# Performance work log

Measured on AMD Instinct MI355X. Metric: run time of the kernel, lower is better.

The kernel has to match this reference:

```python
import jax, jax.numpy as jnp
import numpy as np


def _gcn_conv(x, W, b, src, dst, dinv, n_nodes):
    # x: [N, Cin], W: [Cin, Cout]. PyG GCNConv: transform then normalized aggregate.
    h = x @ W  # [N, Cout]
    norm = dinv[src] * dinv[dst]  # [E']
    msgs = h[src] * norm[:, None]  # gather + scale, [E', Cout]
    out = jax.ops.segment_sum(msgs, dst, num_segments=n_nodes)
    return out + b


def setup_inputs() -> dict:
    key = jax.random.key(0)
    k1, k2, k3, k4 = jax.random.split(key, 4)
    N, E, C = 100000, 1600000, 128
    x = jax.random.normal(k1, (N, C), dtype=jnp.float32)
    edge_index = jax.random.randint(k2, (2, E), 0, N, dtype=jnp.int32)
    # Glorot-ish scale for square layers
    s = 1.0 / np.sqrt(C)
    W1 = jax.random.normal(k3, (C, C), dtype=jnp.float32) * s
    W2 = jax.random.normal(k4, (C, C), dtype=jnp.float32) * s
    b1 = jnp.zeros((C,), dtype=jnp.float32)
    b2 = jnp.zeros((C,), dtype=jnp.float32)
    return {"x": x, "edge_index": edge_index, "W1": W1, "b1": b1, "W2": W2, "b2": b2}


def reference(x, edge_index, W1, b1, W2, b2):
    n_nodes = x.shape[0]
    # Add self-loops (PyG GCNConv default add_self_loops=True)
    loops = jnp.arange(n_nodes, dtype=edge_index.dtype)
    src = jnp.concatenate([edge_index[0], loops])
    dst = jnp.concatenate([edge_index[1], loops])
    # Symmetric normalization: deg^-1/2 with degree counted at destination
    deg = jax.ops.segment_sum(jnp.ones_like(dst, dtype=x.dtype), dst, num_segments=n_nodes)
    dinv = jnp.where(deg > 0, jax.lax.rsqrt(jnp.maximum(deg, 1e-12)), 0.0)

    h = _gcn_conv(x, W1, b1, src, dst, dinv, n_nodes)
    h = jax.nn.relu(h)
    out = _gcn_conv(h, W2, b2, src, dst, dinv, n_nodes)
    return out
```

## Files before the change

kernel.cpp:

```cpp
#include <hip/hip_runtime.h>

#define CDIM 128
#define BCAP 12288
#define LCAP 10240

typedef __bf16 v8bf __attribute__((ext_vector_type(8)));
typedef float  v4f  __attribute__((ext_vector_type(4)));

__device__ __forceinline__ unsigned short f2bf(float f) {
    unsigned int u = __float_as_uint(f);
    u += 0x7fffu + ((u >> 16) & 1u);
    return (unsigned short)(u >> 16);
}

__global__ __launch_bounds__(256) void k_init_bcur(int* __restrict__ bcur) {
    bcur[threadIdx.x] = threadIdx.x * BCAP;
}

__global__ __launch_bounds__(256) void k_bucket_scatter(const int* __restrict__ src,
                                                        const int* __restrict__ dst,
                                                        int* __restrict__ bcur,
                                                        unsigned int* __restrict__ pairs,
                                                        int E) {
    __shared__ int cnt[256];
    __shared__ int cur[256];
    int t = threadIdx.x;
    cnt[t] = 0;
    __syncthreads();
    int e0 = blockIdx.x * 4096;
    int ds[16];
#pragma unroll
    for (int j = 0; j < 16; j++) {
        int e = e0 + j * 256 + t;
        ds[j] = (e < E) ? dst[e] : -1;
        if (ds[j] >= 0) atomicAdd(&cnt[ds[j] >> 9], 1);
    }
    __syncthreads();
    int c = cnt[t];
    cur[t] = c ? atomicAdd(&bcur[t], c) : 0;
    __syncthreads();
#pragma unroll
    for (int j = 0; j < 16; j++) {
        if (ds[j] >= 0) {
            int e = e0 + j * 256 + t;
            int p = atomicAdd(&cur[ds[j] >> 9], 1);
            pairs[p] = ((unsigned)src[e] << 9) | ((unsigned)ds[j] & 511u);
        }
    }
}

__global__ __launch_bounds__(256) void k_bucket_csr(const unsigned int* __restrict__ pairs,
                                                    const int* __restrict__ bcur,
                                                    int* __restrict__ csr,
                                                    int* __restrict__ rowptr,
                                                    float* __restrict__ dinv,
                                                    int N, int E, int NB) {
    __shared__ int sscan[256];
    __shared__ int deg[512];
    __shared__ int pre[512];
    __shared__ int sums[256];
    __shared__ int csrbuf[LCAP];
    int b = blockIdx.x, t = threadIdx.x;

    int c = (t < NB) ? (bcur[t] - t * BCAP) : 0;
    sscan[t] = c;
    __syncthreads();
    for (int off = 1; off < 256; off <<= 1) {
        int v = (t >= off) ? sscan[t - off] : 0;
        __syncthreads();
        sscan[t] += v;
        __syncthreads();
    }
    int cnt   = bcur[b] - b * BCAP;
    if (cnt > LCAP) cnt = LCAP;
    int gbase = sscan[b] - cnt;
    int nb0   = b << 9;

    deg[t] = 0; deg[t + 256] = 0;
    __syncthreads();
    for (int i = t; i < cnt; i += 256)
        atomicAdd(&deg[pairs[b * BCAP + i] & 511u], 1);
    __syncthreads();

    int d0 = deg[2 * t], d1 = deg[2 * t + 1];
    sums[t] = d0 + d1;
    __syncthreads();
    for (int off = 1; off < 256; off <<= 1) {
        int v = (t >= off) ? sums[t - off] : 0;
        __syncthreads();
        sums[t] += v;
        __syncthreads();
    }
    int eb = sums[t] - (d0 + d1);
    pre[2 * t]     = eb;
    pre[2 * t + 1] = eb + d0;
    __syncthreads();

    for (int l = t; l < 512; l += 256) {
        int g = nb0 + l;
        if (g < N) {
            rowptr[g] = gbase + pre[l];
            dinv[g]   = rsqrtf((float)(deg[l] + 1));
        }
    }
    if (b == 0 && t == 0) rowptr[N] = E;
    __syncthreads();

    for (int i = t; i < cnt; i += 256) {
        unsigned int p = pairs[b * BCAP + i];
        int l = (int)(p & 511u);
        int pos = atomicAdd(&pre[l], 1);
        csrbuf[pos] = (int)(p >> 9);
    }
    __syncthreads();

    for (int i = t; i < cnt; i += 256)
        csr[gbase + i] = csrbuf[i];
}

template<int INBF16>
__global__ __launch_bounds__(256) void k_gemm(const void* __restrict__ Xv,
                                              const float* __restrict__ W,
                                              const float* __restrict__ dinv,
                                              unsigned short* __restrict__ Hb,
                                              int N) {
    __shared__ char sX[64 * 256];
    __shared__ char sW[128 * 256];
    const int tid  = threadIdx.x;
    const int row0 = blockIdx.x * 64;

    if (INBF16) {
        const uint4* Xb = (const uint4*)Xv + (size_t)row0 * 16;
#pragma unroll
        for (int i = 0; i < 4; i++) {
            int q   = i * 256 + tid;
            int row = q >> 4;
            int c   = q & 15;
            uint4 v = make_uint4(0u, 0u, 0u, 0u);
            if (row0 + row < N) v = Xb[q];
            int addr = row * 256 + (((c ^ (row & 7)) << 4));
            *(uint4*)(sX + addr) = v;
        }
    } else {
        const float4* Xb = (const float4*)Xv + (size_t)row0 * 32;
#pragma unroll
        for (int i = 0; i < 8; i++) {
            int q   = i * 256 + tid;
            int row = q >> 5;
            int k4  = q & 31;
            float4 v = make_float4(0.f, 0.f, 0.f, 0.f);
            if (row0 + row < N) v = Xb[q];
            unsigned int lo = (unsigned int)f2bf(v.x) | ((unsigned int)f2bf(v.y) << 16);
            unsigned int hi = (unsigned int)f2bf(v.z) | ((unsigned int)f2bf(v.w) << 16);
            int chunk = k4 >> 1, half = k4 & 1;
            int addr = row * 256 + (((chunk ^ (row & 7)) << 4) | (half << 3));
            *(uint2*)(sX + addr) = make_uint2(lo, hi);
        }
    }
    {
        int kg = tid >> 5;
        int c0 = (tid & 31) * 4;
        unsigned int wp[4][8];
#pragma unroll
        for (int i = 0; i < 16; i++) {
            float4 v = *(const float4*)(W + (size_t)(kg * 16 + i) * CDIM + c0);
            unsigned short b0 = f2bf(v.x), b1 = f2bf(v.y), b2 = f2bf(v.z), b3 = f2bf(v.w);
            int ui = i >> 1;
            if ((i & 1) == 0) {
                wp[0][ui] = b0; wp[1][ui] = b1; wp[2][ui] = b2; wp[3][ui] = b3;
            } else {
                wp[0][ui] |= (unsigned int)b0 << 16;
                wp[1][ui] |= (unsigned int)b1 << 16;
                wp[2][ui] |= (unsigned int)b2 << 16;
                wp[3][ui] |= (unsigned int)b3 << 16;
            }
        }
#pragma unroll
        for (int j = 0; j < 4; j++) {
            int c = c0 + j;
            int base = c * 256;
            int a0 = base + ((((kg * 2) ^ (c & 7)) << 4));
            int a1 = base + ((((kg * 2 + 1) ^ (c & 7)) << 4));
            *(uint4*)(sW + a0) = make_uint4(wp[j][0], wp[j][1], wp[j][2], wp[j][3]);
            *(uint4*)(sW + a1) = make_uint4(wp[j][4], wp[j][5], wp[j][6], wp[j][7]);
        }
    }
    __syncthreads();

    const int l   = tid & 63;
    const int wv  = tid >> 6;
    const int ar  = l & 15;
    const int kg2 = l >> 4;

    v4f acc[8];
#pragma unroll
    for (int ct = 0; ct < 8; ct++) acc[ct] = (v4f){0.f, 0.f, 0.f, 0.f};

#pragma unroll
    for (int ks = 0; ks < 4; ks++) {
        int r = wv * 16 + ar;
        v8bf a = *(const v8bf*)(sX + r * 256 + (((ks * 4 + kg2) ^ (r & 7)) << 4));
#pragma unroll
        for (int ct = 0; ct < 8; ct++) {
            int c = ct * 16 + ar;
            v8bf b = *(const v8bf*)(sW + c * 256 + (((ks * 4 + kg2) ^ (c & 7)) << 4));
            acc[ct] = __builtin_amdgcn_mfma_f32_16x16x32_bf16(a, b, acc[ct], 0, 0, 0);
        }
    }

    int rbase = row0 + wv * 16 + kg2 * 4;
#pragma unroll
    for (int reg = 0; reg < 4; reg++) {
        int g = rbase + reg;
        if (g < N) {
            float di = dinv[g];
            unsigned short* orow = Hb + (size_t)g * CDIM;
#pragma unroll
            for (int ct = 0; ct < 8; ct++)
                orow[ct * 16 + ar] = f2bf(acc[ct][reg] * di);
        }
    }
}

template<int OUTBF16>
__global__ __launch_bounds__(256) void k_gather(const unsigned short* __restrict__ Hb,
                                                const int* __restrict__ csr,
                                                const int* __restrict__ rowptr,
                                                const float* __restrict__ dinv,
                                                const float* __restrict__ bias,
                                                void* __restrict__ outv,
                                                int N, int do_relu) {
    int t    = blockIdx.x * 256 + threadIdx.x;
    int n    = t >> 4;
    int lane = t & 15;
    if (n >= N) return;

    const uint4* base = (const uint4*)Hb;
    float acc[8] = {0.f, 0.f, 0.f, 0.f, 0.f, 0.f, 0.f, 0.f};

    auto accum = [&](uint4 u) {
        acc[0] += __uint_as_float(u.x << 16);
        acc[1] += __uint_as_float(u.x & 0xffff0000u);
        acc[2] += __uint_as_float(u.y << 16);
        acc[3] += __uint_as_float(u.y & 0xffff0000u);
        acc[4] += __uint_as_float(u.z << 16);
        acc[5] += __uint_as_float(u.z & 0xffff0000u);
        acc[6] += __uint_as_float(u.w << 16);
        acc[7] += __uint_as_float(u.w & 0xffff0000u);
    };

    int e  = rowptr[n];
    int e1 = rowptr[n + 1];

    accum(base[(size_t)n * 16 + lane]);

    for (; e + 8 <= e1; e += 8) {
        int s0 = csr[e],     s1 = csr[e + 1], s2 = csr[e + 2], s3 = csr[e + 3];
        int s4 = csr[e + 4], s5 = csr[e + 5], s6 = csr[e + 6], s7 = csr[e + 7];
        uint4 u0 = base[(size_t)s0 * 16 + lane];
        uint4 u1 = base[(size_t)s1 * 16 + lane];
        uint4 u2 = base[(size_t)s2 * 16 + lane];
        uint4 u3 = base[(size_t)s3 * 16 + lane];
        uint4 u4 = base[(size_t)s4 * 16 + lane];
        uint4 u5 = base[(size_t)s5 * 16 + lane];
        uint4 u6 = base[(size_t)s6 * 16 + lane];
        uint4 u7 = base[(size_t)s7 * 16 + lane];
        accum(u0); accum(u1); accum(u2); accum(u3);
        accum(u4); accum(u5); accum(u6); accum(u7);
    }
    for (; e + 2 <= e1; e += 2) {
        int s0 = csr[e], s1 = csr[e + 1];
        uint4 u0 = base[(size_t)s0 * 16 + lane];
        uint4 u1 = base[(size_t)s1 * 16 + lane];
        accum(u0); accum(u1);
    }
    if (e < e1) accum(base[(size_t)csr[e] * 16 + lane]);

    float di = dinv[n];
    const float* bp = bias + lane * 8;
    float o[8];
#pragma unroll
    for (int j = 0; j < 8; j++) o[j] = fmaf(acc[j], di, bp[j]);
    if (do_relu) {
#pragma unroll
        for (int j = 0; j < 8; j++) o[j] = fmaxf(o[j], 0.f);
    }

    if (OUTBF16) {
        uint4 u;
        u.x = (unsigned int)f2bf(o[0]) | ((unsigned int)f2bf(o[1]) << 16);
        u.y = (unsigned int)f2bf(o[2]) | ((unsigned int)f2bf(o[3]) << 16);
        u.z = (unsigned int)f2bf(o[4]) | ((unsigned int)f2bf(o[5]) << 16);
        u.w = (unsigned int)f2bf(o[6]) | ((unsigned int)f2bf(o[7]) << 16);
        ((uint4*)outv)[(size_t)n * 16 + lane] = u;
    } else {
        float* op = (float*)outv + (size_t)n * CDIM + lane * 8;
        *(float4*)(op)     = make_float4(o[0], o[1], o[2], o[3]);
        *(float4*)(op + 4) = make_float4(o[4], o[5], o[6], o[7]);
    }
}

extern "C" void kernel_launch(void* const* d_in, const int* in_sizes, int n_in,
                              void* d_out, int out_size, void* d_ws, size_t ws_size,
                              hipStream_t stream) {
    const float* x  = (const float*)d_in[0];
    const int*   ei = (const int*)d_in[1];
    const float* W1 = (const float*)d_in[2];
    const float* b1 = (const float*)d_in[3];
    const float* W2 = (const float*)d_in[4];
    const float* b2 = (const float*)d_in[5];
    float* out = (float*)d_out;

    const int N = in_sizes[0] / CDIM;
    const int E = in_sizes[1] / 2;
    const int* src = ei;
    const int* dst = ei + E;

    char* w = (char*)d_ws;
    unsigned short* Hb = (unsigned short*)w;  w += ((size_t)N * CDIM * 2 + 255) & ~255ull;
    float* dinv   = (float*)w;                w += ((size_t)N * 4 + 255) & ~255ull;
    int*   rowptr = (int*)w;                  w += ((size_t)(N + 1) * 4 + 255) & ~255ull;
    int*   bcur   = (int*)w;                  w += 1024;
    int*   csr    = (int*)w;                  w += ((size_t)E * 4 + 255) & ~255ull;
    unsigned int* pairs = (unsigned int*)w;
    unsigned short* Act = (unsigned short*)w;

    int NB = (N + 511) >> 9;
    int nA = (E + 4095) >> 12;
    int gb = (N + 63) / 64;
    int ga = (int)(((size_t)N * 16 + 255) / 256);

    k_init_bcur<<<1, 256, 0, stream>>>(bcur);
    k_bucket_scatter<<<nA, 256, 0, stream>>>(src, dst, bcur, pairs, E);
    k_bucket_csr<<<NB, 256, 0, stream>>>(pairs, bcur, csr, rowptr, dinv, N, E, NB);

    k_gemm<0><<<gb, 256, 0, stream>>>(x, W1, dinv, Hb, N);
    k_gather<1><<<ga, 256, 0, stream>>>(Hb, csr, rowptr, dinv, b1, Act, N, 1);

    k_gemm<1><<<gb, 256, 0, stream>>>(Act, W2, dinv, Hb, N);
    k_gather<0><<<ga, 256, 0, stream>>>(Hb, csr, rowptr, dinv, b2, out, N, 0);
}
```

Before: 217.1 us.

## Fuse layer-1 aggregation with layer-2 GEMM and pre-convert W2 to bf16

The first aggregation kernel now also performs the second layer's dense transform. Each 16-node block aggregates neighbours, applies bias and ReLU, stages the bf16 row in shared memory, and multiplies by a pre-swizzled bf16 copy of W2 with MFMA. The init kernel builds the W2 bf16 copy. This removes the intermediate activation write/read and one kernel launch. In exchange, every small block reloads the full 32KB W2 tile into shared memory, which raises L2 traffic and reduces occupancy for the latency-bound gather.

```diff
diff --git a/kernel.cpp b/kernel.cpp
--- a/kernel.cpp
+++ b/kernel.cpp
@@ -13,8 +13,25 @@
     return (unsigned short)(u >> 16);
 }
 
-__global__ __launch_bounds__(256) void k_init_bcur(int* __restrict__ bcur) {
-    bcur[threadIdx.x] = threadIdx.x * BCAP;
+__global__ __launch_bounds__(256) void k_init(int* __restrict__ bcur,
+                                              const float* __restrict__ W2,
+                                              uint4* __restrict__ W2bf) {
+    int t = threadIdx.x;
+    if (blockIdx.x == 0) {
+        bcur[t] = t * BCAP;
+        return;
+    }
+    int i  = (blockIdx.x - 1) * 256 + t;
+    int c  = i >> 4;
+    int ch = i & 15;
+    unsigned int p[4];
+#pragma unroll
+    for (int u = 0; u < 4; u++) {
+        float f0 = W2[(size_t)(ch * 8 + 2 * u) * CDIM + c];
+        float f1 = W2[(size_t)(ch * 8 + 2 * u + 1) * CDIM + c];
+        p[u] = (unsigned int)f2bf(f0) | ((unsigned int)f2bf(f1) << 16);
+    }
+    W2bf[(c * 256 + ((ch ^ (c & 7)) << 4)) >> 4] = make_uint4(p[0], p[1], p[2], p[3]);
 }
 
 __global__ __launch_bounds__(256) void k_bucket_scatter(const int* __restrict__ src,
@@ -118,8 +135,7 @@
         csr[gbase + i] = csrbuf[i];
 }
 
-template<int INBF16>
-__global__ __launch_bounds__(256) void k_gemm(const void* __restrict__ Xv,
+__global__ __launch_bounds__(256) void k_gemm(const float* __restrict__ X,
                                               const float* __restrict__ W,
                                               const float* __restrict__ dinv,
                                               unsigned short* __restrict__ Hb,
@@ -129,20 +145,8 @@
     const int tid  = threadIdx.x;
     const int row0 = blockIdx.x * 64;
 
-    if (INBF16) {
-        const uint4* Xb = (const uint4*)Xv + (size_t)row0 * 16;
-#pragma unroll
-        for (int i = 0; i < 4; i++) {
-            int q   = i * 256 + tid;
-            int row = q >> 4;
-            int c   = q & 15;
-            uint4 v = make_uint4(0u, 0u, 0u, 0u);
-            if (row0 + row < N) v = Xb[q];
-            int addr = row * 256 + (((c ^ (row & 7)) << 4));
-            *(uint4*)(sX + addr) = v;
-        }
-    } else {
-        const float4* Xb = (const float4*)Xv + (size_t)row0 * 32;
+    {
+        const float4* Xb = (const float4*)X + (size_t)row0 * 32;
 #pragma unroll
         for (int i = 0; i < 8; i++) {
             int q   = i * 256 + tid;
@@ -222,22 +226,29 @@
     }
 }
 
-template<int OUTBF16>
-__global__ __launch_bounds__(256) void k_gather(const unsigned short* __restrict__ Hb,
-                                                const int* __restrict__ csr,
-                                                const int* __restrict__ rowptr,
-                                                const float* __restrict__ dinv,
-                                                const float* __restrict__ bias,
-                                                void* __restrict__ outv,
-                                                int N, int do_relu) {
-    int t    = blockIdx.x * 256 + threadIdx.x;
-    int n    = t >> 4;
-    int lane = t & 15;
-    if (n >= N) return;
+__global__ __launch_bounds__(256) void k_gather_gemm(const unsigned short* __restrict__ Hb,
+                                                     const int* __restrict__ csr,
+                                                     const int* __restrict__ rowptr,
+                                                     const float* __restrict__ dinv,
+                                                     const float* __restrict__ bias,
+                                                     const uint4* __restrict__ W2bf,
+                                                     unsigned short* __restrict__ Hb2,
+                                                     int N) {
+    __shared__ char sA[16 * 256];
+    __shared__ char sW[128 * 256];
+    const int tid = threadIdx.x;
+    const int n0  = blockIdx.x * 16;
+
+#pragma unroll
+    for (int i = 0; i < 8; i++)
+        *(uint4*)(sW + ((i * 256 + tid) << 4)) = W2bf[i * 256 + tid];
+
+    int n    = n0 + (tid >> 4);
+    int lane = tid & 15;
+    int g    = tid >> 4;
 
     const uint4* base = (const uint4*)Hb;
     float acc[8] = {0.f, 0.f, 0.f, 0.f, 0.f, 0.f, 0.f, 0.f};
-
     auto accum = [&](uint4 u) {
         acc[0] += __uint_as_float(u.x << 16);
         acc[1] += __uint_as_float(u.x & 0xffff0000u);
@@ -249,11 +260,106 @@
         acc[7] += __uint_as_float(u.w & 0xffff0000u);
     };
 
+    uint4 row;
+    if (n < N) {
+        int e  = rowptr[n];
+        int e1 = rowptr[n + 1];
+        accum(base[(size_t)n * 16 + lane]);
+        for (; e + 8 <= e1; e += 8) {
+            int s0 = csr[e],     s1 = csr[e + 1], s2 = csr[e + 2], s3 = csr[e + 3];
+            int s4 = csr[e + 4], s5 = csr[e + 5], s6 = csr[e + 6], s7 = csr[e + 7];
+            uint4 u0 = base[(size_t)s0 * 16 + lane];
+            uint4 u1 = base[(size_t)s1 * 16 + lane];
+            uint4 u2 = base[(size_t)s2 * 16 + lane];
+            uint4 u3 = base[(size_t)s3 * 16 + lane];
+            uint4 u4 = base[(size_t)s4 * 16 + lane];
+            uint4 u5 = base[(size_t)s5 * 16 + lane];
+            uint4 u6 = base[(size_t)s6 * 16 + lane];
+            uint4 u7 = base[(size_t)s7 * 16 + lane];
+            accum(u0); accum(u1); accum(u2); accum(u3);
+            accum(u4); accum(u5); accum(u6); accum(u7);
+        }
+        for (; e + 2 <= e1; e += 2) {
+            int s0 = csr[e], s1 = csr[e + 1];
+            uint4 u0 = base[(size_t)s0 * 16 + lane];
+            uint4 u1 = base[(size_t)s1 * 16 + lane];
+            accum(u0); accum(u1);
+        }
+        if (e < e1) accum(base[(size_t)csr[e] * 16 + lane]);
+
+        float di = dinv[n];
+        const float* bp = bias + lane * 8;
+        float o[8];
+#pragma unroll
+        for (int j = 0; j < 8; j++) o[j] = fmaxf(fmaf(acc[j], di, bp[j]), 0.f);
+        row.x = (unsigned int)f2bf(o[0]) | ((unsigned int)f2bf(o[1]) << 16);
+        row.y = (unsigned int)f2bf(o[2]) | ((unsigned int)f2bf(o[3]) << 16);
+        row.z = (unsigned int)f2bf(o[4]) | ((unsigned int)f2bf(o[5]) << 16);
+        row.w = (unsigned int)f2bf(o[6]) | ((unsigned int)f2bf(o[7]) << 16);
+    } else {
+        row = make_uint4(0u, 0u, 0u, 0u);
+    }
+    *(uint4*)(sA + g * 256 + ((lane ^ (g & 7)) << 4)) = row;
+    __syncthreads();
+
+    const int l   = tid & 63;
+    const int wv  = tid >> 6;
+    const int ar  = l & 15;
+    const int kg2 = l >> 4;
+
+    v4f d0 = (v4f){0.f, 0.f, 0.f, 0.f};
+    v4f d1 = (v4f){0.f, 0.f, 0.f, 0.f};
+    const int c0 = (wv * 2) * 16 + ar;
+    const int c1 = (wv * 2 + 1) * 16 + ar;
+#pragma unroll
+    for (int ks = 0; ks < 4; ks++) {
+        int kc = ks * 4 + kg2;
+        v8bf a  = *(const v8bf*)(sA + ar * 256 + ((kc ^ (ar & 7)) << 4));
+        v8bf b0 = *(const v8bf*)(sW + c0 * 256 + ((kc ^ (c0 & 7)) << 4));
+        v8bf b1 = *(const v8bf*)(sW + c1 * 256 + ((kc ^ (c1 & 7)) << 4));
+        d0 = __builtin_amdgcn_mfma_f32_16x16x32_bf16(a, b0, d0, 0, 0, 0);
+        d1 = __builtin_amdgcn_mfma_f32_16x16x32_bf16(a, b1, d1, 0, 0, 0);
+    }
+#pragma unroll
+    for (int reg = 0; reg < 4; reg++) {
+        int gn = n0 + kg2 * 4 + reg;
+        if (gn < N) {
+            float di = dinv[gn];
+            unsigned short* orow = Hb2 + (size_t)gn * CDIM;
+            orow[c0] = f2bf(d0[reg] * di);
+            orow[c1] = f2bf(d1[reg] * di);
+        }
+    }
+}
+
+__global__ __launch_bounds__(256) void k_gather(const unsigned short* __restrict__ Hb,
+                                                const int* __restrict__ csr,
+                                                const int* __restrict__ rowptr,
+                                                const float* __restrict__ dinv,
+                                                const float* __restrict__ bias,
+                                                float* __restrict__ out,
+                                                int N) {
+    int t    = blockIdx.x * 256 + threadIdx.x;
+    int n    = t >> 4;
+    int lane = t & 15;
+    if (n >= N) return;
+
+    const uint4* base = (const uint4*)Hb;
+    float acc[8] = {0.f, 0.f, 0.f, 0.f, 0.f, 0.f, 0.f, 0.f};
+    auto accum = [&](uint4 u) {
+        acc[0] += __uint_as_float(u.x << 16);
+        acc[1] += __uint_as_float(u.x & 0xffff0000u);
+        acc[2] += __uint_as_float(u.y << 16);
+        acc[3] += __uint_as_float(u.y & 0xffff0000u);
+        acc[4] += __uint_as_float(u.z << 16);
+        acc[5] += __uint_as_float(u.z & 0xffff0000u);
+        acc[6] += __uint_as_float(u.w << 16);
+        acc[7] += __uint_as_float(u.w & 0xffff0000u);
+    };
+
     int e  = rowptr[n];
     int e1 = rowptr[n + 1];
-
     accum(base[(size_t)n * 16 + lane]);
-
     for (; e + 8 <= e1; e += 8) {
         int s0 = csr[e],     s1 = csr[e + 1], s2 = csr[e + 2], s3 = csr[e + 3];
         int s4 = csr[e + 4], s5 = csr[e + 5], s6 = csr[e + 6], s7 = csr[e + 7];
@@ -278,26 +384,14 @@
 
     float di = dinv[n];
     const float* bp = bias + lane * 8;
-    float o[8];
-#pragma unroll
-    for (int j = 0; j < 8; j++) o[j] = fmaf(acc[j], di, bp[j]);
-    if (do_relu) {
-#pragma unroll
-        for (int j = 0; j < 8; j++) o[j] = fmaxf(o[j], 0.f);
-    }
-
-    if (OUTBF16) {
-        uint4 u;
-        u.x = (unsigned int)f2bf(o[0]) | ((unsigned int)f2bf(o[1]) << 16);
-        u.y = (unsigned int)f2bf(o[2]) | ((unsigned int)f2bf(o[3]) << 16);
-        u.z = (unsigned int)f2bf(o[4]) | ((unsigned int)f2bf(o[5]) << 16);
-        u.w = (unsigned int)f2bf(o[6]) | ((unsigned int)f2bf(o[7]) << 16);
-        ((uint4*)outv)[(size_t)n * 16 + lane] = u;
-    } else {
-        float* op = (float*)outv + (size_t)n * CDIM + lane * 8;
-        *(float4*)(op)     = make_float4(o[0], o[1], o[2], o[3]);
-        *(float4*)(op + 4) = make_float4(o[4], o[5], o[6], o[7]);
-    }
+    float* op = out + (size_t)n * CDIM + lane * 8;
+    float4 o0, o1;
+    o0.x = fmaf(acc[0], di, bp[0]); o0.y = fmaf(acc[1], di, bp[1]);
+    o0.z = fmaf(acc[2], di, bp[2]); o0.w = fmaf(acc[3], di, bp[3]);
+    o1.x = fmaf(acc[4], di, bp[4]); o1.y = fmaf(acc[5], di, bp[5]);
+    o1.z = fmaf(acc[6], di, bp[6]); o1.w = fmaf(acc[7], di, bp[7]);
+    *(float4*)(op)     = o0;
+    *(float4*)(op + 4) = o1;
 }
 
 extern "C" void kernel_launch(void* const* d_in, const int* in_sizes, int n_in,
@@ -321,22 +415,23 @@
     float* dinv   = (float*)w;                w += ((size_t)N * 4 + 255) & ~255ull;
     int*   rowptr = (int*)w;                  w += ((size_t)(N + 1) * 4 + 255) & ~255ull;
     int*   bcur   = (int*)w;                  w += 1024;
+    uint4* W2bf   = (uint4*)w;                w += 32768;
     int*   csr    = (int*)w;                  w += ((size_t)E * 4 + 255) & ~255ull;
     unsigned int* pairs = (unsigned int*)w;
-    unsigned short* Act = (unsigned short*)w;
+    unsigned short* Hb2 = (unsigned short*)w;
 
     int NB = (N + 511) >> 9;
     int nA = (E + 4095) >> 12;
     int gb = (N + 63) / 64;
+    int gg = (N + 15) / 16;
     int ga = (int)(((size_t)N * 16 + 255) / 256);
 
-    k_init_bcur<<<1, 256, 0, stream>>>(bcur);
+    k_init<<<9, 256, 0, stream>>>(bcur, W2, W2bf);
     k_bucket_scatter<<<nA, 256, 0, stream>>>(src, dst, bcur, pairs, E);
     k_bucket_csr<<<NB, 256, 0, stream>>>(pairs, bcur, csr, rowptr, dinv, N, E, NB);
 
-    k_gemm<0><<<gb, 256, 0, stream>>>(x, W1, dinv, Hb, N);
-    k_gather<1><<<ga, 256, 0, stream>>>(Hb, csr, rowptr, dinv, b1, Act, N, 1);
-
-    k_gemm<1><<<gb, 256, 0, stream>>>(Act, W2, dinv, Hb, N);
-    k_gather<0><<<ga, 256, 0, stream>>>(Hb, csr, rowptr, dinv, b2, out, N, 0);
-}
+    k_gemm<<<gb, 256, 0, stream>>>(x, W1, dinv, Hb, N);
+    k_gather_gemm<<<gg, 256, 0, stream>>>(Hb, csr, rowptr, dinv, b1, W2bf, Hb2, N);
+
+    k_gather<<<ga, 256, 0, stream>>>(Hb2, csr, rowptr, dinv, b2, out, N);
+}
```

Result: faster. 210.3 us (median of 2 runs) (-3.1%).
